# Kernel tuning notes

Measured on AMD Instinct MI355X. Metric: run time of the kernel, lower is better.

## Reference

```python
import jax, jax.numpy as jnp
import numpy as np

B, N, IN_DIM, D, H = 8, 2048, 256, 512, 4
HD = D // H
GX, GY = 8, 8
IMG_W, IMG_H = 256.0, 256.0
CW, CH = IMG_W / GX, IMG_H / GY
NBH = 1
EPS = 1e-5


def setup_inputs() -> dict:
    key = jax.random.key(0)
    ks = jax.random.split(key, 12)
    s = 0.02
    rn = lambda k, sh: jax.random.normal(k, sh, jnp.float32) * s
    return {
        'features': jax.random.normal(ks[0], (B, N, IN_DIM), jnp.float32),
        'coords': jax.random.uniform(ks[1], (B, N, 2), jnp.float32) * IMG_W,
        'W_feat': rn(ks[2], (IN_DIM, D)), 'b_feat': jnp.zeros((D,), jnp.float32),
        'W_p1': rn(ks[3], (2, D // 2)), 'b_p1': jnp.zeros((D // 2,), jnp.float32),
        'W_p2': rn(ks[4], (D // 2, D)), 'b_p2': jnp.zeros((D,), jnp.float32),
        'Wq': rn(ks[5], (D, D)), 'bq': jnp.zeros((D,), jnp.float32),
        'Wk': rn(ks[6], (D, D)), 'bk': jnp.zeros((D,), jnp.float32),
        'Wv': rn(ks[7], (D, D)), 'bv': jnp.zeros((D,), jnp.float32),
        'Wo': rn(ks[8], (D, D)), 'bo': jnp.zeros((D,), jnp.float32),
        'gamma': jnp.ones((D,), jnp.float32), 'beta': jnp.zeros((D,), jnp.float32),
    }


def reference(features, coords, W_feat, b_feat, W_p1, b_p1, W_p2, b_p2,
              Wq, bq, Wk, bk, Wv, bv, Wo, bo, gamma, beta):
    feat = features @ W_feat + b_feat                          # [B,N,D]
    # --- grid bucketing (mean feature per occupied cell) ---
    gx = jnp.clip((coords[..., 0] / CW).astype(jnp.int32), 0, GX - 1)
    gy = jnp.clip((coords[..., 1] / CH).astype(jnp.int32), 0, GY - 1)
    cell = gx * GY + gy                                        # [B,N]
    G = GX * GY
    seg = (jnp.arange(B, dtype=jnp.int32)[:, None] * G + cell).reshape(-1)
    sums = jax.ops.segment_sum(feat.reshape(B * N, D), seg, num_segments=B * G)
    counts = jax.ops.segment_sum(jnp.ones((B * N,), jnp.float32), seg, num_segments=B * G)
    mean = (sums / jnp.maximum(counts, 1.0)[:, None]).reshape(B, G, D)
    counts = counts.reshape(B, G)
    # --- neighbor cells (static 3x3 window for neighborhood=1) ---
    offs = np.array([(dx, dy) for dx in range(-NBH, NBH + 1) for dy in range(-NBH, NBH + 1)], np.int32)
    K = offs.shape[0]
    pe = jnp.asarray(offs, jnp.float32)
    pe = jax.nn.relu(pe @ W_p1 + b_p1) @ W_p2 + b_p2           # [K,D] pos enc of offsets
    ngx = gx[..., None] + offs[:, 0]                           # [B,N,K]
    ngy = gy[..., None] + offs[:, 1]
    inb = (ngx >= 0) & (ngx < GX) & (ngy >= 0) & (ngy < GY)
    nidx = jnp.clip(ngx, 0, GX - 1) * GY + jnp.clip(ngy, 0, GY - 1)
    bidx = jnp.arange(B)[:, None, None]
    valid = inb & (counts[bidx, nidx] > 0)                     # [B,N,K]
    keys = mean[bidx, nidx] + pe                               # [B,N,K,D]
    # --- per-point attention over <=9 neighbor cells ---
    q = (feat @ Wq + bq).reshape(B, N, H, HD)
    k = (keys @ Wk + bk).reshape(B, N, K, H, HD)
    v = (keys @ Wv + bv).reshape(B, N, K, H, HD)
    scores = jnp.einsum('bnhd,bnkhd->bnhk', q, k) / np.float32(np.sqrt(HD))
    scores = jnp.where(valid[:, :, None, :], scores, jnp.float32(-1e9))
    attn = jax.nn.softmax(scores, axis=-1)
    agg = jnp.einsum('bnhk,bnkhd->bnhd', attn, v).reshape(B, N, D) @ Wo + bo
    enhanced = feat + agg                                      # residual (dropout in eval = identity)
    mu = enhanced.mean(-1, keepdims=True)
    var = enhanced.var(-1, keepdims=True)
    return (enhanced - mu) / jnp.sqrt(var + EPS) * gamma + beta
```

## Files before the change

### kernel.cpp

```cpp
#include <hip/hip_runtime.h>
#include <stdint.h>

typedef unsigned short u16;
typedef unsigned int u32;
typedef __bf16 bf16x8 __attribute__((ext_vector_type(8)));
typedef float f32x4 __attribute__((ext_vector_type(4)));

#define NBATCH 8
#define NPT    2048
#define NPTS   16384
#define INDIM  256
#define DD     512
#define GG     64

__device__ __forceinline__ u16 f2bf(float f){
  u32 u = __builtin_bit_cast(u32, f);
  u += 0x7fffu + ((u >> 16) & 1u);
  return (u16)(u >> 16);
}
__device__ __forceinline__ float bf2f(u16 h){
  u32 u = ((u32)h) << 16;
  return __builtin_bit_cast(float, u);
}
__device__ __forceinline__ void load8(const float* __restrict__ p, float* r){
  float4 a = *(const float4*)p;
  float4 b = *(const float4*)(p + 4);
  r[0]=a.x;r[1]=a.y;r[2]=a.z;r[3]=a.w;r[4]=b.x;r[5]=b.y;r[6]=b.z;r[7]=b.w;
}
__device__ __forceinline__ void load8bf(const u16* __restrict__ p, float* r){
  uint4 v = *(const uint4*)p;
  r[0]=bf2f((u16)v.x); r[1]=bf2f((u16)(v.x>>16));
  r[2]=bf2f((u16)v.y); r[3]=bf2f((u16)(v.y>>16));
  r[4]=bf2f((u16)v.z); r[5]=bf2f((u16)(v.z>>16));
  r[6]=bf2f((u16)v.w); r[7]=bf2f((u16)(v.w>>16));
}
__device__ __forceinline__ void store8(float* __restrict__ p, const float* r){
  float4 a; a.x=r[0];a.y=r[1];a.z=r[2];a.w=r[3];
  float4 b; b.x=r[4];b.y=r[5];b.z=r[6];b.w=r[7];
  *(float4*)p = a; *(float4*)(p+4) = b;
}
__device__ __forceinline__ uint4 pack8(const float* a){
  uint4 pk;
  pk.x = (u32)f2bf(a[0]) | ((u32)f2bf(a[1]) << 16);
  pk.y = (u32)f2bf(a[2]) | ((u32)f2bf(a[3]) << 16);
  pk.z = (u32)f2bf(a[4]) | ((u32)f2bf(a[5]) << 16);
  pk.w = (u32)f2bf(a[6]) | ((u32)f2bf(a[7]) << 16);
  return pk;
}
typedef __attribute__((address_space(1))) unsigned as1u;
typedef __attribute__((address_space(3))) unsigned as3u;
__device__ __forceinline__ void gload16(const void* g, void* l){
  __builtin_amdgcn_global_load_lds((as1u*)(uintptr_t)g, (as3u*)(uintptr_t)l, 16, 0, 0);
}

__device__ __forceinline__ void transpose64(const float* __restrict__ src, int scols,
                                            u16* __restrict__ dst, int dcols,
                                            int r0, int c0, char* smem, int t){
  float (*sh)[65] = (float(*)[65])smem;
  #pragma unroll
  for (int i = 0; i < 16; i++){
    int idx = i*256 + t;
    int r = idx >> 6, c = idx & 63;
    sh[r][c] = src[(size_t)(r0 + r)*scols + c0 + c];
  }
  __syncthreads();
  #pragma unroll
  for (int i = 0; i < 8; i++){
    int idx = i*512 + t*2;
    int oR = idx >> 6, oC = idx & 63;
    u32 pk = (u32)f2bf(sh[oC][oR]) | ((u32)f2bf(sh[oC+1][oR]) << 16);
    *(u32*)(dst + (size_t)(c0 + oR)*dcols + r0 + oC) = pk;
  }
}

#define P_R1 2048
#define P_R2 2112
#define P_R3 2368
#define P_R4 2400
#define P_R5 2409
#define P_R6 2411
#define P_R7 2415
#define P_NB 2423
__global__ __launch_bounds__(256) void prep_kernel(
    const float* __restrict__ features, const float* __restrict__ W_feat,
    const float* __restrict__ Wq, const float* __restrict__ Wk,
    const float* __restrict__ Wv, const float* __restrict__ Wo,
    const float* __restrict__ W_p1, const float* __restrict__ b_p1,
    const float* __restrict__ W_p2, const float* __restrict__ b_p2,
    const float* __restrict__ b_feat, const float* __restrict__ bq,
    const float* __restrict__ bk, const float* __restrict__ bv,
    const float* __restrict__ coords,
    u16* __restrict__ featA, u16* __restrict__ W_feat_bf,
    u16* __restrict__ WqkvT, u16* __restrict__ WoT, u16* __restrict__ WcatT,
    u16* __restrict__ peD, float* __restrict__ bfq, float* __restrict__ biaskv,
    int* __restrict__ order, int* __restrict__ counts, int* __restrict__ cellstart)
{
  __shared__ __align__(16) char smem[34048];
  int bid = blockIdx.x, t = threadIdx.x;
  if (bid < P_R1){
    int i = bid*256 + t;
    float r[8]; load8(features + (size_t)i*8, r);
    *(uint4*)(featA + (size_t)i*8) = pack8(r);
  } else if (bid < P_R2){
    int i = (bid - P_R1)*256 + t;
    float r[8]; load8(W_feat + (size_t)i*8, r);
    *(uint4*)(W_feat_bf + (size_t)i*8) = pack8(r);
  } else if (bid < P_R3){
    int rel = bid - P_R2;
    int mat = rel >> 6, tile = rel & 63;
    int r0 = (tile >> 3)*64, c0 = (tile & 7)*64;
    const float* src = mat==0 ? Wq : (mat==1 ? Wk : (mat==2 ? Wv : Wo));
    u16* dst = mat==0 ? WqkvT : (mat==1 ? WqkvT + (size_t)512*DD
                     : (mat==2 ? WqkvT + (size_t)1024*DD : WoT));
    transpose64(src, DD, dst, DD, r0, c0, smem, t);
  } else if (bid < P_R4){
    int rel = bid - P_R3;
    int r0 = (rel >> 3)*64, c0 = (rel & 7)*64;
    transpose64(W_feat, DD, WcatT, INDIM, r0, c0, smem, t);
  } else if (bid < P_R5){
    int kk = bid - P_R4;
    float dx = (float)(kk/3 - 1), dy = (float)(kk%3 - 1);
    float* h = (float*)smem;
    float hv = dx*W_p1[t] + dy*W_p1[256 + t] + b_p1[t];
    h[t] = hv > 0.f ? hv : 0.f;
    __syncthreads();
    float acc0 = b_p2[t], acc1 = b_p2[t + 256];
    for (int c = 0; c < 256; c++){
      float hc = h[c];
      acc0 += hc * W_p2[(size_t)c*DD + t];
      acc1 += hc * W_p2[(size_t)c*DD + t + 256];
    }
    peD[(size_t)kk*DD + t]       = f2bf(acc0);
    peD[(size_t)kk*DD + t + 256] = f2bf(acc1);
  } else if (bid < P_R6){
    int i = (bid - P_R5)*256 + t;
    float* bfs = (float*)smem;
    bfs[t] = b_feat[t]; bfs[t + 256] = b_feat[t + 256];
    __syncthreads();
    float acc = 0.f;
    for (int k = 0; k < DD; k++) acc += bfs[k] * Wq[(size_t)k*DD + i];
    bfq[i] = acc + bq[i];
  } else if (bid < P_R7){
    int n = (bid - P_R6)*256 + t;
    float* bfs = (float*)smem;
    bfs[t] = b_feat[t]; bfs[t + 256] = b_feat[t + 256];
    __syncthreads();
    const float* W = (n < 512) ? Wk : Wv;
    int c = n & 511;
    float acc = 0.f;
    for (int k = 0; k < DD; k++) acc += bfs[k] * W[(size_t)k*DD + c];
    biaskv[n] = acc + ((n < 512) ? bk[c] : bv[c]);
  } else {
    int b = bid - P_R7;
    u16 (*hist)[65] = (u16(*)[65])smem;
    int* tot  = (int*)(smem + 33280);
    int* base = (int*)(smem + 33536);
    #pragma unroll
    for (int i = 0; i < 65; i++) hist[t][i] = 0;
    int myc[8];
    float cxy[16];
    load8(coords + (size_t)(b*NPT + t*8)*2,     cxy);
    load8(coords + (size_t)(b*NPT + t*8)*2 + 8, cxy + 8);
    #pragma unroll
    for (int i = 0; i < 8; i++){
      int gx = (int)(cxy[2*i]   * (1.0f/32.0f)); gx = gx < 0 ? 0 : (gx > 7 ? 7 : gx);
      int gy = (int)(cxy[2*i+1] * (1.0f/32.0f)); gy = gy < 0 ? 0 : (gy > 7 ? 7 : gy);
      myc[i] = gx*8 + gy;
      hist[t][myc[i]]++;
    }
    __syncthreads();
    if (t < GG){
      int acc = 0;
      for (int tt = 0; tt < 256; tt++){ int v = hist[tt][t]; hist[tt][t] = (u16)acc; acc += v; }
      tot[t] = acc;
    }
    __syncthreads();
    if (t == 0){
      int acc = 0;
      for (int g = 0; g < GG; g++){ base[g] = acc; acc += tot[g]; }
    }
    __syncthreads();
    if (t < GG){
      counts[b*GG + t] = tot[t];
      cellstart[b*GG + t] = base[t];
    }
    #pragma unroll
    for (int i = 0; i < 8; i++){
      int g = myc[i];
      int local = 0;
      #pragma unroll
      for (int j = 0; j < 8; j++) local += (j < i && myc[j] == g) ? 1 : 0;
      order[b*NPT + base[g] + (int)hist[t][g] + local] = t*8 + i;
    }
  }
}

#define BM 128
#define BN 128
#define GEMM_PIPE(Aptr, Btptr, Kv, GXv, NWGv, UIDX)                                \
  __shared__ __align__(16) u16 lA[2][BM*32];                                       \
  __shared__ __align__(16) u16 lB[2][BN*32];                                       \
  int tid = threadIdx.x;                                                           \
  int orig_ = (UIDX);                                                              \
  int swz_ = (orig_ & 7)*((NWGv) >> 3) + (orig_ >> 3);                             \
  int m0 = (swz_ / (GXv)) * BM, n0 = (swz_ % (GXv)) * BN;                          \
  int lane = tid & 63;                                                             \
  int wv = tid >> 6;                                                               \
  int wm = (wv >> 1) * 64, wn = (wv & 1) * 64;                                     \
  int lr = lane & 15;                                                              \
  int kg = (lane >> 4) << 3;                                                       \
  f32x4 acc[4][4] = {};                                                            \
  {                                                                                \
    int srow = lane >> 2;                                                          \
    int scol = (lane & 3) << 3;                                                    \
    const u16* gA0 = (Aptr)  + (size_t)(m0 + wv*32 + srow)*(Kv) + scol;            \
    const u16* gB0 = (Btptr) + (size_t)(n0 + wv*32 + srow)*(Kv) + scol;            \
    int lofs = (wv*32)*32;                                                         \
    int steps = (Kv) >> 5;                                                         \
    gload16(gA0,                   lA[0] + lofs);                                  \
    gload16(gA0 + (size_t)16*(Kv), lA[0] + lofs + 16*32);                          \
    gload16(gB0,                   lB[0] + lofs);                                  \
    gload16(gB0 + (size_t)16*(Kv), lB[0] + lofs + 16*32);                          \
    __syncthreads();                                                               \
    for (int s = 0; s < steps; s++){                                               \
      int cur = s & 1;                                                             \
      if (s + 1 < steps){                                                          \
        int kt = (s + 1) << 5;                                                     \
        gload16(gA0 + kt,                   lA[cur^1] + lofs);                     \
        gload16(gA0 + kt + (size_t)16*(Kv), lA[cur^1] + lofs + 16*32);             \
        gload16(gB0 + kt,                   lB[cur^1] + lofs);                     \
        gload16(gB0 + kt + (size_t)16*(Kv), lB[cur^1] + lofs + 16*32);             \
      }                                                                            \
      bf16x8 af[4], bfv[4];                                                        \
      _Pragma("unroll")                                                            \
      for (int i = 0; i < 4; i++) af[i]  = *(const bf16x8*)&lA[cur][(wm + i*16 + lr)*32 + kg]; \
      _Pragma("unroll")                                                            \
      for (int j = 0; j < 4; j++) bfv[j] = *(const bf16x8*)&lB[cur][(wn + j*16 + lr)*32 + kg]; \
      _Pragma("unroll")                                                            \
      for (int i = 0; i < 4; i++)                                                  \
        _Pragma("unroll")                                                          \
        for (int j = 0; j < 4; j++)                                                \
          acc[i][j] = __builtin_amdgcn_mfma_f32_16x16x32_bf16(af[i], bfv[j], acc[i][j], 0, 0, 0); \
      __syncthreads();                                                             \
    }                                                                              \
  }                                                                                \
  int lrow = (lane >> 4) << 2;

__global__ __launch_bounds__(256) void mid_kernel(
    const u16* __restrict__ WqkvT, const u16* __restrict__ W_feat_bf,
    const u16* __restrict__ peD, u16* __restrict__ Xout, float* __restrict__ meanKV,
    const u16* __restrict__ featA, const int* __restrict__ order,
    const int* __restrict__ counts, const int* __restrict__ cellstart,
    u16* __restrict__ meanF)
{
  if (blockIdx.x < 24){
    GEMM_PIPE(WqkvT, W_feat_bf, 512, 2, 24, (int)blockIdx.x)
    #pragma unroll
    for (int j = 0; j < 4; j++){
      int col = n0 + wn + j*16 + lr;
      #pragma unroll
      for (int i = 0; i < 4; i++){
        int row0 = m0 + wm + i*16 + lrow;
        #pragma unroll
        for (int r = 0; r < 4; r++)
          Xout[(size_t)(row0 + r)*INDIM + col] = f2bf(acc[i][j][r]);
      }
    }
  } else if (blockIdx.x < 60){
    __shared__ float pesh[512];
    int bid2 = blockIdx.x - 24;
    int kk = bid2 >> 2, seg = bid2 & 3;
    int t = threadIdx.x;
    int n = seg*256 + t;
    pesh[t]       = bf2f(peD[(size_t)kk*DD + t]);
    pesh[t + 256] = bf2f(peD[(size_t)kk*DD + t + 256]);
    __syncthreads();
    const u16* wrow = WqkvT + (size_t)(512 + n)*DD;
    float acc = 0.f;
    for (int d8 = 0; d8 < 64; d8++){
      float w8[8]; load8bf(wrow + d8*8, w8);
      #pragma unroll
      for (int j = 0; j < 8; j++) acc += pesh[d8*8 + j]*w8[j];
    }
    meanKV[(size_t)(512 + kk)*1024 + n] = acc;
  } else {
    __shared__ float part[128][2];
    int bg = blockIdx.x - 60;
    int b = bg >> 6;
    int t = threadIdx.x;
    int p = t & 127, half = t >> 7;
    int cnt = counts[bg], start = cellstart[bg];
    const int* ord = order + b*NPT + start;
    float a0 = 0.f, a1 = 0.f;
    for (int n = half; n < cnt; n += 2){
      u32 v = *(const u32*)(featA + (((size_t)(b*NPT + ord[n])) << 8) + p*2);
      a0 += bf2f((u16)v); a1 += bf2f((u16)(v >> 16));
    }
    if (half){ part[p][0] = a0; part[p][1] = a1; }
    __syncthreads();
    if (!half){
      a0 += part[p][0]; a1 += part[p][1];
      float inv = 1.f / (float)(cnt > 0 ? cnt : 1);
      *(u32*)(meanF + (size_t)bg*INDIM + p*2) =
          (u32)f2bf(a0*inv) | ((u32)f2bf(a1*inv) << 16);
    }
  }
}

__global__ __launch_bounds__(256) void featq_kernel(
    const u16* __restrict__ featA, const u16* __restrict__ WcatT,
    const u16* __restrict__ meanF, const u16* __restrict__ WfkvT,
    const float* __restrict__ bias0, const float* __restrict__ bias1,
    const float* __restrict__ biaskv,
    u16* __restrict__ feat_bf, u16* __restrict__ q_bf, float* __restrict__ meanKV)
{
  int isMean = blockIdx.x >= 1024;
  const u16* A  = isMean ? meanF : featA;
  const u16* Bt = isMean ? WfkvT : WcatT;
  int uidx = isMean ? ((int)blockIdx.x - 1024) : (int)blockIdx.x;
  int NWG  = isMean ? 32 : 1024;
  GEMM_PIPE(A, Bt, 256, 8, NWG, uidx)
  if (!isMean){
    int half = n0 >> 9;
    u16* outp = half ? q_bf : feat_bf;
    const float* bias = half ? bias1 : bias0;
    int nb = n0 & 511;
    #pragma unroll
    for (int j = 0; j < 4; j++){
      int col = nb + wn + j*16 + lr;
      float bcol = bias[col];
      #pragma unroll
      for (int i = 0; i < 4; i++){
        int row0 = m0 + wm + i*16 + lrow;
        #pragma unroll
        for (int r = 0; r < 4; r++)
          outp[(size_t)(row0 + r)*DD + col] = f2bf(acc[i][j][r] + bcol);
      }
    }
  } else {
    #pragma unroll
    for (int j = 0; j < 4; j++){
      int col = n0 + wn + j*16 + lr;
      float bcol = biaskv[col];
      #pragma unroll
      for (int i = 0; i < 4; i++){
        int row0 = m0 + wm + i*16 + lrow;
        #pragma unroll
        for (int r = 0; r < 4; r++)
          meanKV[(size_t)(row0 + r)*1024 + col] = acc[i][j][r] + bcol;
      }
    }
  }
}

__global__ __launch_bounds__(1024) void attn_cells(
    const u16* __restrict__ q, const float* __restrict__ meanKV,
    const int* __restrict__ order, const int* __restrict__ counts,
    const int* __restrict__ cellstart, u16* __restrict__ agg)
{
  int bg = blockIdx.x;
  int b = bg >> 6, c = bg & 63;
  int gx = c >> 3, gy = c & 7;
  __shared__ __align__(16) u16 Kf[9][DD];
  __shared__ __align__(16) u16 Vf[9][DD];
  __shared__ int vrow[9];
  int t = threadIdx.x;
  if (t < 9){
    int dx = t/3 - 1, dy = t%3 - 1;
    int nx = gx + dx, ny = gy + dy;
    int inb = ((unsigned)nx < 8u) && ((unsigned)ny < 8u);
    int row = b*GG + (((nx&7) << 3) | (ny&7));
    vrow[t] = (inb && counts[row] > 0) ? row : -1;
  }
  __syncthreads();
  int d = 2*(t & 255);
  for (int kk = (t >> 8); kk < 9; kk += 4){
    int row = vrow[kk];
    if (row >= 0){
      float2 mk = *(const float2*)&meanKV[(size_t)row*1024 + d];
      float2 pk = *(const float2*)&meanKV[(size_t)(512+kk)*1024 + d];
      float2 mv = *(const float2*)&meanKV[(size_t)row*1024 + 512 + d];
      float2 pv = *(const float2*)&meanKV[(size_t)(512+kk)*1024 + 512 + d];
      *(u32*)&Kf[kk][d] = (u32)f2bf(mk.x+pk.x) | ((u32)f2bf(mk.y+pk.y) << 16);
      *(u32*)&Vf[kk][d] = (u32)f2bf(mv.x+pv.x) | ((u32)f2bf(mv.y+pv.y) << 16);
    }
  }
  __syncthreads();
  int cnt = counts[bg];
  int wv = t >> 6, lane = t & 63;
  const int* ord = order + b*NPT + cellstart[bg];
  for (int i = wv; i < cnt; i += 16){
    size_t p = (size_t)b*NPT + ord[i];
    float qv[8];
    load8bf(q + p*DD + lane*8, qv);
    float s[9];
    #pragma unroll
    for (int kk = 0; kk < 9; kk++){
      float partial = 0.f;
      if (vrow[kk] >= 0){
        float kv[8]; load8bf(&Kf[kk][lane*8], kv);
        #pragma unroll
        for (int j = 0; j < 8; j++) partial += qv[j]*kv[j];
      }
      partial += __shfl_xor(partial, 1);
      partial += __shfl_xor(partial, 2);
      partial += __shfl_xor(partial, 4);
      partial += __shfl_xor(partial, 8);
      s[kk] = (vrow[kk] >= 0) ? partial * 0.08838834764831843f : -1e30f;
    }
    float mx = s[0];
    #pragma unroll
    for (int kk = 1; kk < 9; kk++) mx = fmaxf(mx, s[kk]);
    float w[9], sum = 0.f;
    #pragma unroll
    for (int kk = 0; kk < 9; kk++){
      w[kk] = (vrow[kk] >= 0) ? __expf(s[kk] - mx) : 0.f;
      sum += w[kk];
    }
    float inv = 1.f / sum;
    float a[8] = {0,0,0,0,0,0,0,0};
    #pragma unroll
    for (int kk = 0; kk < 9; kk++){
      if (vrow[kk] >= 0){
        float wk = w[kk] * inv;
        float vv[8]; load8bf(&Vf[kk][lane*8], vv);
        #pragma unroll
        for (int j = 0; j < 8; j++) a[j] += wk*vv[j];
      }
    }
    *(uint4*)&agg[p*DD + lane*8] = pack8(a);
  }
}

__global__ __launch_bounds__(256) void lin_kernel(
    const u16* __restrict__ agg_bf, const u16* __restrict__ WoT,
    const float* __restrict__ bo, u16* __restrict__ lin_bf)
{
  GEMM_PIPE(agg_bf, WoT, 512, 4, 512, (int)blockIdx.x)
  #pragma unroll
  for (int j = 0; j < 4; j++){
    int col = n0 + wn + j*16 + lr;
    float bcol = bo[col];
    #pragma unroll
    for (int i = 0; i < 4; i++){
      int row0 = m0 + wm + i*16 + lrow;
      #pragma unroll
      for (int r = 0; r < 4; r++)
        lin_bf[(size_t)(row0 + r)*DD + col] = f2bf(acc[i][j][r] + bcol);
    }
  }
}

__global__ __launch_bounds__(256) void ln_kernel(
    const u16* __restrict__ feat, const u16* __restrict__ lin,
    const float* __restrict__ gamma, const float* __restrict__ beta,
    float* __restrict__ out)
{
  int wv = threadIdx.x >> 6, lane = threadIdx.x & 63;
  size_t r = (size_t)blockIdx.x * 4 + wv;
  int d0 = lane * 8;
  float fv[8], lv[8];
  load8bf(feat + r*DD + d0, fv);
  load8bf(lin  + r*DD + d0, lv);
  float e[8], s1 = 0.f, s2 = 0.f;
  #pragma unroll
  for (int j = 0; j < 8; j++){ e[j] = fv[j] + lv[j]; s1 += e[j]; s2 += e[j]*e[j]; }
  #pragma unroll
  for (int m = 1; m < 64; m <<= 1){ s1 += __shfl_xor(s1, m); s2 += __shfl_xor(s2, m); }
  float mu  = s1 * (1.f/512.f);
  float var = s2 * (1.f/512.f) - mu*mu;
  float istd = rsqrtf(var + 1e-5f);
  float gv[8], bev[8];
  load8(gamma + d0, gv); load8(beta + d0, bev);
  float o[8];
  #pragma unroll
  for (int j = 0; j < 8; j++) o[j] = (e[j] - mu)*istd*gv[j] + bev[j];
  store8(out + r*DD + d0, o);
}

extern "C" void kernel_launch(void* const* d_in, const int* in_sizes, int n_in,
                              void* d_out, int out_size, void* d_ws, size_t ws_size,
                              hipStream_t stream) {
  (void)in_sizes; (void)n_in; (void)out_size; (void)ws_size;
  const float* features = (const float*)d_in[0];
  const float* coords   = (const float*)d_in[1];
  const float* W_feat   = (const float*)d_in[2];
  const float* b_feat   = (const float*)d_in[3];
  const float* W_p1     = (const float*)d_in[4];
  const float* b_p1     = (const float*)d_in[5];
  const float* W_p2     = (const float*)d_in[6];
  const float* b_p2     = (const float*)d_in[7];
  const float* Wq = (const float*)d_in[8];  const float* bq = (const float*)d_in[9];
  const float* Wk = (const float*)d_in[10]; const float* bk = (const float*)d_in[11];
  const float* Wv = (const float*)d_in[12]; const float* bv = (const float*)d_in[13];
  const float* Wo = (const float*)d_in[14]; const float* bo = (const float*)d_in[15];
  const float* gamma = (const float*)d_in[16]; const float* beta = (const float*)d_in[17];
  float* out = (float*)d_out;

  char* ws = (char*)d_ws;
  size_t off = 0;
  auto alloc = [&](size_t bytes) -> void* {
    void* p = ws + off;
    off = (off + bytes + 255) & ~(size_t)255;
    return p;
  };
  u16*   featA     = (u16*)  alloc((size_t)NPTS*INDIM*2);
  u16*   feat_bf   = (u16*)  alloc((size_t)NPTS*DD*2);
  u16*   q_bf      = (u16*)  alloc((size_t)NPTS*DD*2);
  u16*   agg_bf    = (u16*)  alloc((size_t)NPTS*DD*2);
  u16*   lin_bf    = (u16*)  alloc((size_t)NPTS*DD*2);
  u16*   W_feat_bf = (u16*)  alloc((size_t)INDIM*DD*2);
  u16*   WqkvT     = (u16*)  alloc((size_t)1536*DD*2);
  u16*   WoT       = (u16*)  alloc((size_t)DD*DD*2);
  u16*   WcatT     = (u16*)  alloc((size_t)1024*INDIM*2);
  u16*   WfkvT     = (u16*)  alloc((size_t)1024*INDIM*2);
  u16*   peD       = (u16*)  alloc((size_t)9*DD*2);
  u16*   meanF     = (u16*)  alloc((size_t)512*INDIM*2);
  float* meanKV    = (float*)alloc((size_t)640*1024*4);
  float* bfq       = (float*)alloc((size_t)DD*4);
  float* biaskv    = (float*)alloc((size_t)1024*4);
  int*   order     = (int*)  alloc((size_t)NPTS*4);
  int*   counts    = (int*)  alloc((size_t)NBATCH*GG*4);
  int*   cellstart = (int*)  alloc((size_t)NBATCH*GG*4);
  u16*   Xout      = WcatT + (size_t)512*INDIM;

  prep_kernel<<<P_NB, 256, 0, stream>>>(
      features, W_feat, Wq, Wk, Wv, Wo, W_p1, b_p1, W_p2, b_p2,
      b_feat, bq, bk, bv, coords,
      featA, W_feat_bf, WqkvT, WoT, WcatT, peD, bfq, biaskv,
      order, counts, cellstart);
  mid_kernel<<<572, 256, 0, stream>>>(
      WqkvT, W_feat_bf, peD, Xout, meanKV, featA, order, counts, cellstart, meanF);
  featq_kernel<<<1056, 256, 0, stream>>>(
      featA, WcatT, meanF, WfkvT, b_feat, bfq, biaskv, feat_bf, q_bf, meanKV);
  attn_cells<<<NBATCH*GG, 1024, 0, stream>>>(q_bf, meanKV, order, counts, cellstart, agg_bf);
  lin_kernel<<<512, 256, 0, stream>>>(agg_bf, WoT, bo, lin_bf);
  ln_kernel<<<NPTS/4, 256, 0, stream>>>(feat_bf, lin_bf, gamma, beta, out);
}
```

Measured before the change: 108.9 us.

## Move feat GEMM into mid kernel and stage GEMM epilogues through LDS

The feature projection GEMM (featA @ W_feat) moves from the later featq kernel into mid_kernel, where it runs alongside the Wqkv-fold, pos-encoding and cell-mean blocks, since it does not depend on them. The remaining kernel now computes only q (from the folded weight) and the mean-KV projection. GEMM epilogues now write bf16 tiles to a padded LDS buffer and store them with 16-byte coalesced writes instead of scattered 2-byte stores. Shared memory becomes one unified buffer, and workspace buffers are rearranged so WfqT and WfkvT alias Xout.

```diff
diff --git a/kernel.cpp b/kernel.cpp
--- a/kernel.cpp
+++ b/kernel.cpp
@@ -197,10 +197,9 @@
 
 #define BM 128
 #define BN 128
-#define GEMM_PIPE(Aptr, Btptr, Kv, GXv, NWGv, UIDX)                                \
-  __shared__ __align__(16) u16 lA[2][BM*32];                                       \
-  __shared__ __align__(16) u16 lB[2][BN*32];                                       \
-  int tid = threadIdx.x;                                                           \
+#define GEMM_PIPE(SMEMB, Aptr, Btptr, Kv, GXv, NWGv, UIDX)                         \
+  u16* lA_ = (u16*)(SMEMB);                                                        \
+  u16* lB_ = (u16*)((char*)(SMEMB) + 16384);                                       \
   int orig_ = (UIDX);                                                              \
   int swz_ = (orig_ & 7)*((NWGv) >> 3) + (orig_ >> 3);                             \
   int m0 = (swz_ / (GXv)) * BM, n0 = (swz_ % (GXv)) * BN;                          \
@@ -217,25 +216,29 @@
     const u16* gB0 = (Btptr) + (size_t)(n0 + wv*32 + srow)*(Kv) + scol;            \
     int lofs = (wv*32)*32;                                                         \
     int steps = (Kv) >> 5;                                                         \
-    gload16(gA0,                   lA[0] + lofs);                                  \
-    gload16(gA0 + (size_t)16*(Kv), lA[0] + lofs + 16*32);                          \
-    gload16(gB0,                   lB[0] + lofs);                                  \
-    gload16(gB0 + (size_t)16*(Kv), lB[0] + lofs + 16*32);                          \
+    gload16(gA0,                   lA_ + lofs);                                    \
+    gload16(gA0 + (size_t)16*(Kv), lA_ + lofs + 512);                              \
+    gload16(gB0,                   lB_ + lofs);                                    \
+    gload16(gB0 + (size_t)16*(Kv), lB_ + lofs + 512);                              \
     __syncthreads();                                                               \
     for (int s = 0; s < steps; s++){                                               \
       int cur = s & 1;                                                             \
+      u16* lAc = lA_ + cur*4096;                                                   \
+      u16* lBc = lB_ + cur*4096;                                                   \
       if (s + 1 < steps){                                                          \
         int kt = (s + 1) << 5;                                                     \
-        gload16(gA0 + kt,                   lA[cur^1] + lofs);                     \
-        gload16(gA0 + kt + (size_t)16*(Kv), lA[cur^1] + lofs + 16*32);             \
-        gload16(gB0 + kt,                   lB[cur^1] + lofs);                     \
-        gload16(gB0 + kt + (size_t)16*(Kv), lB[cur^1] + lofs + 16*32);             \
+        u16* lAn = lA_ + (cur^1)*4096;                                             \
+        u16* lBn = lB_ + (cur^1)*4096;                                             \
+        gload16(gA0 + kt,                   lAn + lofs);                           \
+        gload16(gA0 + kt + (size_t)16*(Kv), lAn + lofs + 512);                     \
+        gload16(gB0 + kt,                   lBn + lofs);                           \
+        gload16(gB0 + kt + (size_t)16*(Kv), lBn + lofs + 512);                     \
       }                                                                            \
       bf16x8 af[4], bfv[4];                                                        \
       _Pragma("unroll")                                                            \
-      for (int i = 0; i < 4; i++) af[i]  = *(const bf16x8*)&lA[cur][(wm + i*16 + lr)*32 + kg]; \
+      for (int i = 0; i < 4; i++) af[i]  = *(const bf16x8*)&lAc[(wm + i*16 + lr)*32 + kg]; \
       _Pragma("unroll")                                                            \
-      for (int j = 0; j < 4; j++) bfv[j] = *(const bf16x8*)&lB[cur][(wn + j*16 + lr)*32 + kg]; \
+      for (int j = 0; j < 4; j++) bfv[j] = *(const bf16x8*)&lBc[(wn + j*16 + lr)*32 + kg]; \
       _Pragma("unroll")                                                            \
       for (int i = 0; i < 4; i++)                                                  \
         _Pragma("unroll")                                                          \
@@ -246,15 +249,42 @@
   }                                                                                \
   int lrow = (lane >> 4) << 2;
 
+#define EPI_BF16(SMEMB, DST, LDN, BIAS)                                            \
+  {                                                                                \
+    u16* Cs = (u16*)(SMEMB);                                                       \
+    _Pragma("unroll")                                                              \
+    for (int j = 0; j < 4; j++){                                                   \
+      int col = wn + j*16 + lr;                                                    \
+      float bcol = (BIAS)[n0 + col];                                               \
+      _Pragma("unroll")                                                            \
+      for (int i = 0; i < 4; i++){                                                 \
+        int r0 = wm + i*16 + lrow;                                                 \
+        _Pragma("unroll")                                                          \
+        for (int r = 0; r < 4; r++)                                                \
+          Cs[(r0 + r)*136 + col] = f2bf(acc[i][j][r] + bcol);                      \
+      }                                                                            \
+    }                                                                              \
+    __syncthreads();                                                               \
+    _Pragma("unroll")                                                              \
+    for (int k = 0; k < 8; k++){                                                   \
+      int idx = k*256 + tid;                                                       \
+      int row = idx >> 4, c8 = (idx & 15) << 3;                                    \
+      *(uint4*)&(DST)[(size_t)(m0 + row)*(LDN) + n0 + c8] = *(uint4*)&Cs[row*136 + c8]; \
+    }                                                                              \
+  }
+
 __global__ __launch_bounds__(256) void mid_kernel(
     const u16* __restrict__ WqkvT, const u16* __restrict__ W_feat_bf,
     const u16* __restrict__ peD, u16* __restrict__ Xout, float* __restrict__ meanKV,
     const u16* __restrict__ featA, const int* __restrict__ order,
     const int* __restrict__ counts, const int* __restrict__ cellstart,
-    u16* __restrict__ meanF)
+    u16* __restrict__ meanF, const u16* __restrict__ WcatT,
+    const float* __restrict__ b_feat, u16* __restrict__ feat_bf)
 {
+  __shared__ __align__(16) char SMEM[34816];
+  int tid = threadIdx.x;
   if (blockIdx.x < 24){
-    GEMM_PIPE(WqkvT, W_feat_bf, 512, 2, 24, (int)blockIdx.x)
+    GEMM_PIPE(SMEM, WqkvT, W_feat_bf, 512, 2, 24, (int)blockIdx.x)
     #pragma unroll
     for (int j = 0; j < 4; j++){
       int col = n0 + wn + j*16 + lr;
@@ -267,13 +297,12 @@
       }
     }
   } else if (blockIdx.x < 60){
-    __shared__ float pesh[512];
+    float* pesh = (float*)SMEM;
     int bid2 = blockIdx.x - 24;
     int kk = bid2 >> 2, seg = bid2 & 3;
-    int t = threadIdx.x;
-    int n = seg*256 + t;
-    pesh[t]       = bf2f(peD[(size_t)kk*DD + t]);
-    pesh[t + 256] = bf2f(peD[(size_t)kk*DD + t + 256]);
+    int n = seg*256 + tid;
+    pesh[tid]       = bf2f(peD[(size_t)kk*DD + tid]);
+    pesh[tid + 256] = bf2f(peD[(size_t)kk*DD + tid + 256]);
     __syncthreads();
     const u16* wrow = WqkvT + (size_t)(512 + n)*DD;
     float acc = 0.f;
@@ -283,12 +312,11 @@
       for (int j = 0; j < 8; j++) acc += pesh[d8*8 + j]*w8[j];
     }
     meanKV[(size_t)(512 + kk)*1024 + n] = acc;
-  } else {
-    __shared__ float part[128][2];
+  } else if (blockIdx.x < 572){
+    float (*part)[2] = (float(*)[2])SMEM;
     int bg = blockIdx.x - 60;
     int b = bg >> 6;
-    int t = threadIdx.x;
-    int p = t & 127, half = t >> 7;
+    int p = tid & 127, half = tid >> 7;
     int cnt = counts[bg], start = cellstart[bg];
     const int* ord = order + b*NPT + start;
     float a0 = 0.f, a1 = 0.f;
@@ -304,40 +332,25 @@
       *(u32*)(meanF + (size_t)bg*INDIM + p*2) =
           (u32)f2bf(a0*inv) | ((u32)f2bf(a1*inv) << 16);
     }
-  }
-}
-
-__global__ __launch_bounds__(256) void featq_kernel(
-    const u16* __restrict__ featA, const u16* __restrict__ WcatT,
+  } else {
+    GEMM_PIPE(SMEM, featA, WcatT, 256, 4, 512, (int)blockIdx.x - 572)
+    EPI_BF16(SMEM, feat_bf, DD, b_feat)
+  }
+}
+
+__global__ __launch_bounds__(256) void qmean_kernel(
+    const u16* __restrict__ featA, const u16* __restrict__ WfqT,
     const u16* __restrict__ meanF, const u16* __restrict__ WfkvT,
-    const float* __restrict__ bias0, const float* __restrict__ bias1,
-    const float* __restrict__ biaskv,
-    u16* __restrict__ feat_bf, u16* __restrict__ q_bf, float* __restrict__ meanKV)
+    const float* __restrict__ bfq, const float* __restrict__ biaskv,
+    u16* __restrict__ q_bf, float* __restrict__ meanKV)
 {
-  int isMean = blockIdx.x >= 1024;
-  const u16* A  = isMean ? meanF : featA;
-  const u16* Bt = isMean ? WfkvT : WcatT;
-  int uidx = isMean ? ((int)blockIdx.x - 1024) : (int)blockIdx.x;
-  int NWG  = isMean ? 32 : 1024;
-  GEMM_PIPE(A, Bt, 256, 8, NWG, uidx)
-  if (!isMean){
-    int half = n0 >> 9;
-    u16* outp = half ? q_bf : feat_bf;
-    const float* bias = half ? bias1 : bias0;
-    int nb = n0 & 511;
-    #pragma unroll
-    for (int j = 0; j < 4; j++){
-      int col = nb + wn + j*16 + lr;
-      float bcol = bias[col];
-      #pragma unroll
-      for (int i = 0; i < 4; i++){
-        int row0 = m0 + wm + i*16 + lrow;
-        #pragma unroll
-        for (int r = 0; r < 4; r++)
-          outp[(size_t)(row0 + r)*DD + col] = f2bf(acc[i][j][r] + bcol);
-      }
-    }
+  __shared__ __align__(16) char SMEM[34816];
+  int tid = threadIdx.x;
+  if (blockIdx.x < 512){
+    GEMM_PIPE(SMEM, featA, WfqT, 256, 4, 512, (int)blockIdx.x)
+    EPI_BF16(SMEM, q_bf, DD, bfq)
   } else {
+    GEMM_PIPE(SMEM, meanF, WfkvT, 256, 8, 32, (int)blockIdx.x - 512)
     #pragma unroll
     for (int j = 0; j < 4; j++){
       int col = n0 + wn + j*16 + lr;
@@ -436,19 +449,10 @@
     const u16* __restrict__ agg_bf, const u16* __restrict__ WoT,
     const float* __restrict__ bo, u16* __restrict__ lin_bf)
 {
-  GEMM_PIPE(agg_bf, WoT, 512, 4, 512, (int)blockIdx.x)
-  #pragma unroll
-  for (int j = 0; j < 4; j++){
-    int col = n0 + wn + j*16 + lr;
-    float bcol = bo[col];
-    #pragma unroll
-    for (int i = 0; i < 4; i++){
-      int row0 = m0 + wm + i*16 + lrow;
-      #pragma unroll
-      for (int r = 0; r < 4; r++)
-        lin_bf[(size_t)(row0 + r)*DD + col] = f2bf(acc[i][j][r] + bcol);
-    }
-  }
+  __shared__ __align__(16) char SMEM[34816];
+  int tid = threadIdx.x;
+  GEMM_PIPE(SMEM, agg_bf, WoT, 512, 4, 512, (int)blockIdx.x)
+  EPI_BF16(SMEM, lin_bf, DD, bo)
 }
 
 __global__ __launch_bounds__(256) void ln_kernel(
@@ -512,8 +516,8 @@
   u16*   W_feat_bf = (u16*)  alloc((size_t)INDIM*DD*2);
   u16*   WqkvT     = (u16*)  alloc((size_t)1536*DD*2);
   u16*   WoT       = (u16*)  alloc((size_t)DD*DD*2);
-  u16*   WcatT     = (u16*)  alloc((size_t)1024*INDIM*2);
-  u16*   WfkvT     = (u16*)  alloc((size_t)1024*INDIM*2);
+  u16*   WcatT     = (u16*)  alloc((size_t)512*INDIM*2);
+  u16*   Xout      = (u16*)  alloc((size_t)1536*INDIM*2);
   u16*   peD       = (u16*)  alloc((size_t)9*DD*2);
   u16*   meanF     = (u16*)  alloc((size_t)512*INDIM*2);
   float* meanKV    = (float*)alloc((size_t)640*1024*4);
@@ -522,17 +526,19 @@
   int*   order     = (int*)  alloc((size_t)NPTS*4);
   int*   counts    = (int*)  alloc((size_t)NBATCH*GG*4);
   int*   cellstart = (int*)  alloc((size_t)NBATCH*GG*4);
-  u16*   Xout      = WcatT + (size_t)512*INDIM;
+  u16*   WfqT      = Xout;
+  u16*   WfkvT     = Xout + (size_t)512*INDIM;
 
   prep_kernel<<<P_NB, 256, 0, stream>>>(
       features, W_feat, Wq, Wk, Wv, Wo, W_p1, b_p1, W_p2, b_p2,
       b_feat, bq, bk, bv, coords,
       featA, W_feat_bf, WqkvT, WoT, WcatT, peD, bfq, biaskv,
       order, counts, cellstart);
-  mid_kernel<<<572, 256, 0, stream>>>(
-      WqkvT, W_feat_bf, peD, Xout, meanKV, featA, order, counts, cellstart, meanF);
-  featq_kernel<<<1056, 256, 0, stream>>>(
-      featA, WcatT, meanF, WfkvT, b_feat, bfq, biaskv, feat_bf, q_bf, meanKV);
+  mid_kernel<<<1084, 256, 0, stream>>>(
+      WqkvT, W_feat_bf, peD, Xout, meanKV, featA, order, counts, cellstart,
+      meanF, WcatT, b_feat, feat_bf);
+  qmean_kernel<<<544, 256, 0, stream>>>(
+      featA, WfqT, meanF, WfkvT, bfq, biaskv, q_bf, meanKV);
   attn_cells<<<NBATCH*GG, 1024, 0, stream>>>(q_bf, meanKV, order, counts, cellstart, agg_bf);
   lin_kernel<<<512, 256, 0, stream>>>(agg_bf, WoT, bo, lin_bf);
   ln_kernel<<<NPTS/4, 256, 0, stream>>>(feat_bf, lin_bf, gamma, beta, out);
```

Measured after the change: 102.8 us. 5.6% less time.
